# Optimization experiments

Hardware: AMD Instinct MI355X
Metric: run time of the kernel (lower is better)

The kernel has to match this reference:

```python
import jax, jax.numpy as jnp
import numpy as np

V, D, F, B, E = 50257, 1024, 2048, 64, 512  # vocab, embed/rnn dim, fc hidden, batch, entities


def setup_inputs() -> dict:
    key = jax.random.key(0)
    ks = jax.random.split(key, 12)
    s = 0.05
    return {
        "entity_hiddens": jax.random.normal(ks[0], (B, E, D), jnp.float32),
        "question": jax.random.randint(ks[1], (B,), 0, V),
        "keys_mask": jax.random.randint(ks[2], (B, E), 0, 2).astype(bool),
        "emb": jax.random.normal(ks[3], (V, D), jnp.float32) * s,
        "W1": jax.random.normal(ks[4], (D, F), jnp.float32) * s,
        "b1": jnp.zeros((F,), jnp.float32),
        "W2": jax.random.normal(ks[5], (F, D), jnp.float32) * s,
        "b2": jnp.zeros((D,), jnp.float32),
        "A": jax.random.normal(ks[6], (D, D), jnp.float32) * s,  # entity_attn_matrix
        "H": jax.random.normal(ks[7], (D, D), jnp.float32) * s,
        "Ws": jax.random.normal(ks[8], (D, V), jnp.float32) * s,
        "bs": jnp.zeros((V,), jnp.float32),
    }


def reference(entity_hiddens, question, keys_mask, emb, W1, b1, W2, b2, A, H, Ws, bs):
    # embed question token and project: [B, D]
    eq0 = emb[question]
    q = jax.nn.relu(eq0 @ W1 + b1) @ W2 + b2
    # attention_entities actual returned math:
    # reduce_sum(expand_dims(q@A,1) * boolean_mask(entities, mask), axis=1)
    # == (q @ A) * sum over all masked entities (a single [D] vector)
    qA = q @ A  # [B, D]
    m = keys_mask.astype(entity_hiddens.dtype)
    ent_sum = jnp.sum(entity_hiddens * m[..., None], axis=(0, 1))  # [D]
    u = qA * ent_sum  # [B, D]
    logits = (q + u @ H) @ Ws + bs  # [B, V]
    return jax.nn.softmax(logits, axis=-1)
```

## Files before the change

kernel.cpp:

```cpp
#include <hip/hip_runtime.h>
#include <stdint.h>

#define V_ 50257
#define D_ 1024
#define F_ 2048
#define B_ 64
#define E_ 512
#define ROWS_ (B_*E_)

typedef __attribute__((ext_vector_type(8))) short bf16x8;
typedef __attribute__((ext_vector_type(4))) float f32x4;
typedef __attribute__((ext_vector_type(4), aligned(4))) float f32x4a;

__device__ __forceinline__ unsigned rne1(float a) {
  unsigned u = __float_as_uint(a);
  return (u + 0x7FFFu + ((u >> 16) & 1u)) >> 16;
}

__device__ __forceinline__ float waveMax(float v) {
#pragma unroll
  for (int o = 32; o > 0; o >>= 1) v = fmaxf(v, __shfl_xor(v, o, 64));
  return v;
}
__device__ __forceinline__ float waveSum(float v) {
#pragma unroll
  for (int o = 32; o > 0; o >>= 1) v += __shfl_xor(v, o, 64);
  return v;
}


__device__ __forceinline__ void ent_partial_body(int bid, const float* __restrict__ eh,
                                                 const void* __restrict__ mask,
                                                 float* __restrict__ part) {
  __shared__ int s_mode;
  const int tid = threadIdx.x;
  const uint32_t* mu = (const uint32_t*)mask;
  int f = 0;
  for (int i = tid; i < (ROWS_ / 4); i += 256) {
    uint32_t u = mu[i];
    if (u == 0x3F800000u) f |= 2;
    else if (u & 0xFFFFFF00u) f |= 1;
  }
  if (tid == 0) s_mode = 0;
  __syncthreads();
  if (f) atomicOr(&s_mode, f);
  __syncthreads();
  const int sm = s_mode;
  const int mode = (sm & 1) ? 1 : ((sm & 2) ? 2 : 0);

  float4 acc = make_float4(0.f, 0.f, 0.f, 0.f);
  const float4* eh4 = (const float4*)eh;
  for (int row = bid; row < ROWS_; row += 512) {
    bool on;
    if (mode == 1)      on = ((const unsigned char*)mask)[row] != 0;
    else if (mode == 2) on = ((const float*)mask)[row] != 0.f;
    else                on = ((const int*)mask)[row] != 0;
    if (on) {
      float4 v = eh4[(size_t)row * (D_ / 4) + tid];
      acc.x += v.x; acc.y += v.y; acc.z += v.z; acc.w += v.w;
    }
  }
  ((float4*)part)[(size_t)bid * (D_ / 4) + tid] = acc;
}

__device__ __forceinline__ void ent_reduce_body(int bid, const float* __restrict__ part,
                                                float* __restrict__ entsum) {
  int d = bid * 256 + threadIdx.x;
  float s0 = 0.f, s1 = 0.f, s2 = 0.f, s3 = 0.f;
  for (int i = 0; i < 512; i += 4) {
    s0 += part[(size_t)(i    ) * D_ + d];
    s1 += part[(size_t)(i + 1) * D_ + d];
    s2 += part[(size_t)(i + 2) * D_ + d];
    s3 += part[(size_t)(i + 3) * D_ + d];
  }
  entsum[d] = (s0 + s1) + (s2 + s3);
}

__device__ __forceinline__ void gemm64_body(int bx, int by, const float* __restrict__ X,
                                            const int* __restrict__ gatherIdx,
                                            const float* __restrict__ emb,
                                            const float* __restrict__ W,
                                            int K, int N, int KB, float* __restrict__ part) {
  const int l  = threadIdx.x & 63;
  const int rg = __builtin_amdgcn_readfirstlane((int)(threadIdx.x >> 6));
  const int c  = bx * 64 + l;
  const int k0 = by * KB;
  const int m0 = rg * 16;

  const float* Xp = gatherIdx ? emb : X;
  int rb[16];
#pragma unroll
  for (int r = 0; r < 16; ++r) {
    int m = m0 + r;
    rb[r] = gatherIdx ? gatherIdx[m] * K : m * K;
  }

  float acc[16];
#pragma unroll
  for (int r = 0; r < 16; ++r) acc[r] = 0.f;

  for (int k = k0; k < k0 + KB; k += 8) {
    float wv[8];
#pragma unroll
    for (int j = 0; j < 8; ++j) wv[j] = W[(size_t)(k + j) * N + c];
#pragma unroll
    for (int r = 0; r < 16; ++r) {
      float4 x0 = *(const float4*)&Xp[rb[r] + k];
      float4 x1 = *(const float4*)&Xp[rb[r] + k + 4];
      acc[r] = fmaf(x0.x, wv[0], acc[r]);
      acc[r] = fmaf(x0.y, wv[1], acc[r]);
      acc[r] = fmaf(x0.z, wv[2], acc[r]);
      acc[r] = fmaf(x0.w, wv[3], acc[r]);
      acc[r] = fmaf(x1.x, wv[4], acc[r]);
      acc[r] = fmaf(x1.y, wv[5], acc[r]);
      acc[r] = fmaf(x1.z, wv[6], acc[r]);
      acc[r] = fmaf(x1.w, wv[7], acc[r]);
    }
  }
  size_t base = (size_t)by * ((size_t)64 * N);
#pragma unroll
  for (int r = 0; r < 16; ++r) part[base + (size_t)(m0 + r) * N + c] = acc[r];
}

__device__ __forceinline__ void reduce_ep_body(int bid, const float* __restrict__ part,
                                               int nsplit, int MN, int N,
                                               const float* __restrict__ vecB,
                                               const float* __restrict__ addend,
                                               int mode, float* __restrict__ dst,
                                               unsigned short* __restrict__ dhi,
                                               unsigned short* __restrict__ dlo) {
  int idx = bid * 256 + threadIdx.x;
  if (idx >= MN) return;
  float s = 0.f;
  for (int i = 0; i < nsplit; ++i) s += part[(size_t)i * MN + idx];
  int c = idx & (N - 1);
  if (mode == 1)      { s += vecB[c]; s = s > 0.f ? s : 0.f; dst[idx] = s; }
  else if (mode == 2) { s += vecB[c]; dst[idx] = s; }
  else if (mode == 3) { s *= vecB[c]; dst[idx] = s; }
  else {
    s += addend[idx];
    unsigned hi = rne1(s);
    float hif = __uint_as_float(hi << 16);
    dhi[idx] = (unsigned short)hi;
    dlo[idx] = (unsigned short)rne1(s - hif);
  }
}

__global__ void k_p1(const float* __restrict__ eh, const void* __restrict__ mask,
                     float* __restrict__ entpart, const int* __restrict__ ques,
                     const float* __restrict__ emb, const float* __restrict__ W1,
                     float* __restrict__ gpart) {
  int bid = blockIdx.x;
  if (bid < 512) ent_partial_body(bid, eh, mask, entpart);
  else {
    int b2 = bid - 512;
    gemm64_body(b2 & 31, b2 >> 5, nullptr, ques, emb, W1, 1024, 2048, 64, gpart);
  }
}

__global__ void k_p2(const float* __restrict__ entpart, float* __restrict__ entsum,
                     const float* __restrict__ gpart, const float* __restrict__ b1,
                     float* __restrict__ hbuf) {
  int bid = blockIdx.x;
  if (bid < 4) ent_reduce_body(bid, entpart, entsum);
  else reduce_ep_body(bid - 4, gpart, 16, 64 * 2048, 2048, b1, nullptr, 1, hbuf, nullptr, nullptr);
}

__global__ void k_gemm64(const float* __restrict__ X, const float* __restrict__ W,
                         int K, int N, int KB, float* __restrict__ part) {
  gemm64_body(blockIdx.x, blockIdx.y, X, nullptr, nullptr, W, K, N, KB, part);
}

__global__ void k_reduce_ep(const float* __restrict__ part, int nsplit, int MN, int N,
                            const float* __restrict__ vecB, const float* __restrict__ addend,
                            int mode, float* __restrict__ dst,
                            unsigned short* __restrict__ dhi, unsigned short* __restrict__ dlo) {
  reduce_ep_body(blockIdx.x, part, nsplit, MN, N, vecB, addend, mode, dst, dhi, dlo);
}

__global__ __launch_bounds__(512, 1) void k_gemm_big(const unsigned short* __restrict__ zhi,
                                                     const unsigned short* __restrict__ zlo,
                                                     const float* __restrict__ Ws,
                                                     float* __restrict__ part2) {
  __shared__ float lds[2][32 * 516];
  const int t   = threadIdx.x;
  const int l   = t & 63;
  const int w   = t >> 6;
  const int col = l & 15;
  const int g   = l >> 4;
  const int c0  = (blockIdx.x < 98) ? blockIdx.x * 512 : (V_ - 512);
  const int kbase = blockIdx.y * 512;

  const int rr0 = t >> 7;
  const int ccf = (t & 127) * 4;

  unsigned aoff[4];
#pragma unroll
  for (int m = 0; m < 4; ++m) aoff[m] = (unsigned)((m * 16 + col) * D_ + g * 8);

  f32x4 acc[4][4];
#pragma unroll
  for (int n = 0; n < 4; ++n)
#pragma unroll
    for (int m = 0; m < 4; ++m) acc[n][m] = (f32x4){0.f, 0.f, 0.f, 0.f};

  {
    f32x4a gg[8];
#pragma unroll
    for (int r8 = 0; r8 < 8; ++r8) {
      const int r = r8 * 4 + rr0;
      gg[r8] = *(const f32x4a*)(Ws + (size_t)(kbase + r) * V_ + c0 + ccf);
    }
#pragma unroll
    for (int r8 = 0; r8 < 8; ++r8) {
      const int r = r8 * 4 + rr0;
      *(f32x4*)&lds[0][r * 516 + ccf] = (f32x4)gg[r8];
    }
  }
  __syncthreads();

  for (int tt = 0; tt < 16; ++tt) {
    const int buf = tt & 1;
    const int k0  = kbase + tt * 32;

    bf16x8 ah[4], al[4];
#pragma unroll
    for (int m = 0; m < 4; ++m) {
      ah[m] = *(const bf16x8*)(zhi + aoff[m] + k0);
      al[m] = *(const bf16x8*)(zlo + aoff[m] + k0);
    }

    f32x4a gg[8];
    if (tt + 1 < 16) {
      const float* wb = Ws + (size_t)(k0 + 32) * V_ + c0 + ccf;
#pragma unroll
      for (int r8 = 0; r8 < 8; ++r8)
        gg[r8] = *(const f32x4a*)(wb + (size_t)(r8 * 4 + rr0) * V_);
    }
    __builtin_amdgcn_sched_barrier(0);

#pragma unroll
    for (int n = 0; n < 4; ++n) {
      float f[8];
#pragma unroll
      for (int j = 0; j < 8; ++j)
        f[j] = lds[buf][(g * 8 + j) * 516 + w * 64 + n * 16 + col];

      union { bf16x8 v; unsigned u[4]; } bh, bl;
#pragma unroll
      for (int j = 0; j < 4; ++j) {
        unsigned h0 = rne1(f[2 * j]);
        unsigned h1 = rne1(f[2 * j + 1]);
        float h0f = __uint_as_float(h0 << 16);
        float h1f = __uint_as_float(h1 << 16);
        bh.u[j] = h0 | (h1 << 16);
        bl.u[j] = rne1(f[2 * j] - h0f) | (rne1(f[2 * j + 1] - h1f) << 16);
      }
#pragma unroll
      for (int m = 0; m < 4; ++m) acc[n][m] = __builtin_amdgcn_mfma_f32_16x16x32_bf16(ah[m], bh.v, acc[n][m], 0, 0, 0);
#pragma unroll
      for (int m = 0; m < 4; ++m) acc[n][m] = __builtin_amdgcn_mfma_f32_16x16x32_bf16(ah[m], bl.v, acc[n][m], 0, 0, 0);
#pragma unroll
      for (int m = 0; m < 4; ++m) acc[n][m] = __builtin_amdgcn_mfma_f32_16x16x32_bf16(al[m], bh.v, acc[n][m], 0, 0, 0);
    }
    __builtin_amdgcn_sched_barrier(0);

    if (tt + 1 < 16) {
#pragma unroll
      for (int r8 = 0; r8 < 8; ++r8) {
        const int r = r8 * 4 + rr0;
        *(f32x4*)&lds[buf ^ 1][r * 516 + ccf] = (f32x4)gg[r8];
      }
    }
    __syncthreads();
  }

  float* pout = part2 + (size_t)blockIdx.y * ((size_t)64 * V_);
#pragma unroll
  for (int n = 0; n < 4; ++n) {
    const int c = c0 + w * 64 + n * 16 + col;
    if (c < V_) {
#pragma unroll
      for (int m = 0; m < 4; ++m)
#pragma unroll
        for (int i = 0; i < 4; ++i)
          pout[(size_t)(m * 16 + g * 4 + i) * V_ + c] = acc[n][m][i];
    }
  }
}

#define SM_CHUNK 12565

__global__ void k_redbias(const float* __restrict__ part2, const float* __restrict__ bs,
                          float* __restrict__ logits) {
  const int r = blockIdx.x >> 2, q = blockIdx.x & 3;
  const int beg = q * SM_CHUNK;
  const int end = (beg + SM_CHUNK < V_) ? beg + SM_CHUNK : V_;
  const float* p0 = part2 + (size_t)r * V_;
  const float* p1 = part2 + (size_t)64 * V_ + (size_t)r * V_;
  float* orow = logits + (size_t)r * V_;
  for (int i = beg + threadIdx.x; i < end; i += 256) orow[i] = p0[i] + p1[i] + bs[i];
}


__global__ void k_softmax1(const float* __restrict__ logits, float2* __restrict__ stats) {
  __shared__ float smx[4], ssum[4];
  const int r = blockIdx.x >> 2, q = blockIdx.x & 3;
  const int beg = q * SM_CHUNK;
  const int end = (beg + SM_CHUNK < V_) ? beg + SM_CHUNK : V_;
  const float* row = logits + (size_t)r * V_;

  float mx = -3.4e38f;
  for (int i = beg + threadIdx.x; i < end; i += 256) mx = fmaxf(mx, row[i]);
  mx = waveMax(mx);
  if ((threadIdx.x & 63) == 0) smx[threadIdx.x >> 6] = mx;
  __syncthreads();
  mx = fmaxf(fmaxf(smx[0], smx[1]), fmaxf(smx[2], smx[3]));

  float s = 0.f;
  for (int i = beg + threadIdx.x; i < end; i += 256) s += __expf(row[i] - mx);
  s = waveSum(s);
  if ((threadIdx.x & 63) == 0) ssum[threadIdx.x >> 6] = s;
  __syncthreads();
  s = (ssum[0] + ssum[1]) + (ssum[2] + ssum[3]);

  if (threadIdx.x == 0) stats[blockIdx.x] = make_float2(mx, s);
}

__global__ void k_softmax2(const float* __restrict__ logits, const float2* __restrict__ stats,
                           float* __restrict__ out) {
  const int r = blockIdx.x >> 2, q = blockIdx.x & 3;
  float2 s0 = stats[r * 4 + 0], s1 = stats[r * 4 + 1];
  float2 s2 = stats[r * 4 + 2], s3 = stats[r * 4 + 3];
  float M = fmaxf(fmaxf(s0.x, s1.x), fmaxf(s2.x, s3.x));
  float S = s0.y * __expf(s0.x - M) + s1.y * __expf(s1.x - M)
          + s2.y * __expf(s2.x - M) + s3.y * __expf(s3.x - M);
  float inv = 1.f / S;
  const int beg = q * SM_CHUNK;
  const int end = (beg + SM_CHUNK < V_) ? beg + SM_CHUNK : V_;
  const float* row = logits + (size_t)r * V_;
  float* orow = out + (size_t)r * V_;
  for (int i = beg + threadIdx.x; i < end; i += 256) orow[i] = __expf(row[i] - M) * inv;
}

extern "C" void kernel_launch(void* const* d_in, const int* in_sizes, int n_in,
                              void* d_out, int out_size, void* d_ws, size_t ws_size,
                              hipStream_t stream) {
  const float* eh   = (const float*)d_in[0];
  const int*   ques = (const int*)d_in[1];
  const void*  mask = d_in[2];
  const float* emb  = (const float*)d_in[3];
  const float* W1   = (const float*)d_in[4];
  const float* b1   = (const float*)d_in[5];
  const float* W2   = (const float*)d_in[6];
  const float* b2   = (const float*)d_in[7];
  const float* A    = (const float*)d_in[8];
  const float* H    = (const float*)d_in[9];
  const float* Ws   = (const float*)d_in[10];
  const float* bs   = (const float*)d_in[11];
  float* out = (float*)d_out;
  char* ws = (char*)d_ws;

  float*          logits  = (float*)(ws + 0);
  float*          gpart   = (float*)(ws + 0);
  float*          entpart = (float*)(ws + 12866048);
  float*          entsum  = (float*)(ws + 14963200);
  float*          hbuf    = (float*)(ws + 14967296);
  float*          qbuf    = (float*)(ws + 15491584);
  float*          ubuf    = (float*)(ws + 15753728);
  unsigned short* zhi16   = (unsigned short*)(ws + 16015872);
  unsigned short* zlo16   = (unsigned short*)(ws + 16146944);
  float2*         stats   = (float2*)(ws + 16278016);
  float*          part2   = (float*)(ws + 20971520);

  k_p1<<<1024, 256, 0, stream>>>(eh, mask, entpart, ques, emb, W1, gpart);
  k_p2<<<516, 256, 0, stream>>>(entpart, entsum, gpart, b1, hbuf);

  k_gemm64<<<dim3(16, 32), 256, 0, stream>>>(hbuf, W2, 2048, 1024, 64, gpart);
  k_reduce_ep<<<256, 256, 0, stream>>>(gpart, 32, 64 * 1024, 1024, b2, nullptr, 2, qbuf, nullptr, nullptr);

  k_gemm64<<<dim3(16, 16), 256, 0, stream>>>(qbuf, A, 1024, 1024, 64, gpart);
  k_reduce_ep<<<256, 256, 0, stream>>>(gpart, 16, 64 * 1024, 1024, entsum, nullptr, 3, ubuf, nullptr, nullptr);

  k_gemm64<<<dim3(16, 16), 256, 0, stream>>>(ubuf, H, 1024, 1024, 64, gpart);
  k_reduce_ep<<<256, 256, 0, stream>>>(gpart, 16, 64 * 1024, 1024, nullptr, qbuf, 4, nullptr, zhi16, zlo16);

  k_gemm_big<<<dim3(99, 2), 512, 0, stream>>>(zhi16, zlo16, Ws, part2);
  k_redbias<<<256, 256, 0, stream>>>(part2, bs, logits);

  k_softmax1<<<256, 256, 0, stream>>>(logits, stats);
  k_softmax2<<<256, 256, 0, stream>>>(logits, stats, out);

  (void)in_sizes; (void)n_in; (void)out_size; (void)ws_size;
}
```

Baseline: 268.7 us.

## Fuse split-K reduction into softmax, pre-pack A fragments, shrink big GEMM tiles

```diff
diff --git a/kernel.cpp b/kernel.cpp
--- a/kernel.cpp
+++ b/kernel.cpp
@@ -67,6 +67,7 @@
                                                 float* __restrict__ entsum) {
   int d = bid * 256 + threadIdx.x;
   float s0 = 0.f, s1 = 0.f, s2 = 0.f, s3 = 0.f;
+#pragma unroll 8
   for (int i = 0; i < 512; i += 4) {
     s0 += part[(size_t)(i    ) * D_ + d];
     s1 += part[(size_t)(i + 1) * D_ + d];
@@ -122,28 +123,46 @@
   for (int r = 0; r < 16; ++r) part[base + (size_t)(m0 + r) * N + c] = acc[r];
 }
 
-__device__ __forceinline__ void reduce_ep_body(int bid, const float* __restrict__ part,
-                                               int nsplit, int MN, int N,
-                                               const float* __restrict__ vecB,
-                                               const float* __restrict__ addend,
-                                               int mode, float* __restrict__ dst,
-                                               unsigned short* __restrict__ dhi,
-                                               unsigned short* __restrict__ dlo) {
+template<int NSPLIT>
+__device__ __forceinline__ void reduce_body_t(int bid, const float* __restrict__ part,
+                                              int MN, int N,
+                                              const float* __restrict__ vecB,
+                                              const float* __restrict__ addend,
+                                              int mode, float* __restrict__ dst,
+                                              unsigned short* __restrict__ ph,
+                                              unsigned short* __restrict__ pl) {
   int idx = bid * 256 + threadIdx.x;
   if (idx >= MN) return;
+
+  if (mode == 4) {
+    const int d   = idx;
+    const int j   = d & 7;
+    const int l   = (d >> 3) & 63;
+    const int m   = (d >> 9) & 3;
+    const int tg  = d >> 11;
+    const int col = l & 15;
+    const int g   = l >> 4;
+    const int row = m * 16 + col;
+    const int kk  = tg * 32 + g * 8 + j;
+    const int src = row * 1024 + kk;
+    float s = 0.f;
+#pragma unroll
+    for (int i = 0; i < NSPLIT; ++i) s += part[(size_t)i * MN + src];
+    s += addend[src];
+    unsigned hi = rne1(s);
+    float hif = __uint_as_float(hi << 16);
+    ph[d] = (unsigned short)hi;
+    pl[d] = (unsigned short)rne1(s - hif);
+    return;
+  }
+
   float s = 0.f;
-  for (int i = 0; i < nsplit; ++i) s += part[(size_t)i * MN + idx];
+#pragma unroll
+  for (int i = 0; i < NSPLIT; ++i) s += part[(size_t)i * MN + idx];
   int c = idx & (N - 1);
   if (mode == 1)      { s += vecB[c]; s = s > 0.f ? s : 0.f; dst[idx] = s; }
   else if (mode == 2) { s += vecB[c]; dst[idx] = s; }
-  else if (mode == 3) { s *= vecB[c]; dst[idx] = s; }
-  else {
-    s += addend[idx];
-    unsigned hi = rne1(s);
-    float hif = __uint_as_float(hi << 16);
-    dhi[idx] = (unsigned short)hi;
-    dlo[idx] = (unsigned short)rne1(s - hif);
-  }
+  else                { s *= vecB[c]; dst[idx] = s; }
 }
 
 __global__ void k_p1(const float* __restrict__ eh, const void* __restrict__ mask,
@@ -163,7 +182,7 @@
                      float* __restrict__ hbuf) {
   int bid = blockIdx.x;
   if (bid < 4) ent_reduce_body(bid, entpart, entsum);
-  else reduce_ep_body(bid - 4, gpart, 16, 64 * 2048, 2048, b1, nullptr, 1, hbuf, nullptr, nullptr);
+  else reduce_body_t<16>(bid - 4, gpart, 64 * 2048, 2048, b1, nullptr, 1, hbuf, nullptr, nullptr);
 }
 
 __global__ void k_gemm64(const float* __restrict__ X, const float* __restrict__ W,
@@ -171,32 +190,26 @@
   gemm64_body(blockIdx.x, blockIdx.y, X, nullptr, nullptr, W, K, N, KB, part);
 }
 
-__global__ void k_reduce_ep(const float* __restrict__ part, int nsplit, int MN, int N,
-                            const float* __restrict__ vecB, const float* __restrict__ addend,
-                            int mode, float* __restrict__ dst,
-                            unsigned short* __restrict__ dhi, unsigned short* __restrict__ dlo) {
-  reduce_ep_body(blockIdx.x, part, nsplit, MN, N, vecB, addend, mode, dst, dhi, dlo);
-}
-
-__global__ __launch_bounds__(512, 1) void k_gemm_big(const unsigned short* __restrict__ zhi,
-                                                     const unsigned short* __restrict__ zlo,
+template<int NSPLIT>
+__global__ void k_reduce_t(const float* __restrict__ part, int MN, int N,
+                           const float* __restrict__ vecB, const float* __restrict__ addend,
+                           int mode, float* __restrict__ dst,
+                           unsigned short* __restrict__ ph, unsigned short* __restrict__ pl) {
+  reduce_body_t<NSPLIT>(blockIdx.x, part, MN, N, vecB, addend, mode, dst, ph, pl);
+}
+
+__global__ __launch_bounds__(256, 2) void k_gemm_big(const unsigned short* __restrict__ zpkh,
+                                                     const unsigned short* __restrict__ zpkl,
                                                      const float* __restrict__ Ws,
                                                      float* __restrict__ part2) {
-  __shared__ float lds[2][32 * 516];
+  __shared__ float lds[2][32 * 260];
   const int t   = threadIdx.x;
   const int l   = t & 63;
   const int w   = t >> 6;
   const int col = l & 15;
   const int g   = l >> 4;
-  const int c0  = (blockIdx.x < 98) ? blockIdx.x * 512 : (V_ - 512);
+  const int c0  = (blockIdx.x < 196) ? blockIdx.x * 256 : (V_ - 256);
   const int kbase = blockIdx.y * 512;
-
-  const int rr0 = t >> 7;
-  const int ccf = (t & 127) * 4;
-
-  unsigned aoff[4];
-#pragma unroll
-  for (int m = 0; m < 4; ++m) aoff[m] = (unsigned)((m * 16 + col) * D_ + g * 8);
 
   f32x4 acc[4][4];
 #pragma unroll
@@ -207,35 +220,36 @@
   {
     f32x4a gg[8];
 #pragma unroll
-    for (int r8 = 0; r8 < 8; ++r8) {
-      const int r = r8 * 4 + rr0;
-      gg[r8] = *(const f32x4a*)(Ws + (size_t)(kbase + r) * V_ + c0 + ccf);
-    }
-#pragma unroll
-    for (int r8 = 0; r8 < 8; ++r8) {
-      const int r = r8 * 4 + rr0;
-      *(f32x4*)&lds[0][r * 516 + ccf] = (f32x4)gg[r8];
+    for (int i = 0; i < 8; ++i) {
+      const int r = w + 4 * i;
+      gg[i] = *(const f32x4a*)(Ws + (size_t)(kbase + r) * V_ + c0 + 4 * l);
+    }
+#pragma unroll
+    for (int i = 0; i < 8; ++i) {
+      const int r = w + 4 * i;
+      *(f32x4*)&lds[0][r * 260 + 4 * l] = (f32x4)gg[i];
     }
   }
   __syncthreads();
 
   for (int tt = 0; tt < 16; ++tt) {
     const int buf = tt & 1;
-    const int k0  = kbase + tt * 32;
+    const int tg  = (kbase >> 5) + tt;
 
     bf16x8 ah[4], al[4];
 #pragma unroll
     for (int m = 0; m < 4; ++m) {
-      ah[m] = *(const bf16x8*)(zhi + aoff[m] + k0);
-      al[m] = *(const bf16x8*)(zlo + aoff[m] + k0);
+      const int zb = ((tg * 4 + m) * 64 + l) * 8;
+      ah[m] = *(const bf16x8*)(zpkh + zb);
+      al[m] = *(const bf16x8*)(zpkl + zb);
     }
 
     f32x4a gg[8];
     if (tt + 1 < 16) {
-      const float* wb = Ws + (size_t)(k0 + 32) * V_ + c0 + ccf;
-#pragma unroll
-      for (int r8 = 0; r8 < 8; ++r8)
-        gg[r8] = *(const f32x4a*)(wb + (size_t)(r8 * 4 + rr0) * V_);
+      const float* wb = Ws + (size_t)(kbase + (tt + 1) * 32) * V_ + c0 + 4 * l;
+#pragma unroll
+      for (int i = 0; i < 8; ++i)
+        gg[i] = *(const f32x4a*)(wb + (size_t)(w + 4 * i) * V_);
     }
     __builtin_amdgcn_sched_barrier(0);
 
@@ -244,7 +258,7 @@
       float f[8];
 #pragma unroll
       for (int j = 0; j < 8; ++j)
-        f[j] = lds[buf][(g * 8 + j) * 516 + w * 64 + n * 16 + col];
+        f[j] = lds[buf][(g * 8 + j) * 260 + w * 64 + n * 16 + col];
 
       union { bf16x8 v; unsigned u[4]; } bh, bl;
 #pragma unroll
@@ -267,9 +281,9 @@
 
     if (tt + 1 < 16) {
 #pragma unroll
-      for (int r8 = 0; r8 < 8; ++r8) {
-        const int r = r8 * 4 + rr0;
-        *(f32x4*)&lds[buf ^ 1][r * 516 + ccf] = (f32x4)gg[r8];
+      for (int i = 0; i < 8; ++i) {
+        const int r = w + 4 * i;
+        *(f32x4*)&lds[buf ^ 1][r * 260 + 4 * l] = (f32x4)gg[i];
       }
     }
     __syncthreads();
@@ -279,46 +293,34 @@
 #pragma unroll
   for (int n = 0; n < 4; ++n) {
     const int c = c0 + w * 64 + n * 16 + col;
-    if (c < V_) {
-#pragma unroll
-      for (int m = 0; m < 4; ++m)
-#pragma unroll
-        for (int i = 0; i < 4; ++i)
-          pout[(size_t)(m * 16 + g * 4 + i) * V_ + c] = acc[n][m][i];
-    }
+#pragma unroll
+    for (int m = 0; m < 4; ++m)
+#pragma unroll
+      for (int i = 0; i < 4; ++i)
+        pout[(size_t)(m * 16 + g * 4 + i) * V_ + c] = acc[n][m][i];
   }
 }
 
 #define SM_CHUNK 12565
 
-__global__ void k_redbias(const float* __restrict__ part2, const float* __restrict__ bs,
-                          float* __restrict__ logits) {
+__global__ void k_softmax1(const float* __restrict__ part2, const float* __restrict__ bs,
+                           float2* __restrict__ stats) {
+  __shared__ float smx[4], ssum[4];
   const int r = blockIdx.x >> 2, q = blockIdx.x & 3;
   const int beg = q * SM_CHUNK;
   const int end = (beg + SM_CHUNK < V_) ? beg + SM_CHUNK : V_;
   const float* p0 = part2 + (size_t)r * V_;
   const float* p1 = part2 + (size_t)64 * V_ + (size_t)r * V_;
-  float* orow = logits + (size_t)r * V_;
-  for (int i = beg + threadIdx.x; i < end; i += 256) orow[i] = p0[i] + p1[i] + bs[i];
-}
-
-
-__global__ void k_softmax1(const float* __restrict__ logits, float2* __restrict__ stats) {
-  __shared__ float smx[4], ssum[4];
-  const int r = blockIdx.x >> 2, q = blockIdx.x & 3;
-  const int beg = q * SM_CHUNK;
-  const int end = (beg + SM_CHUNK < V_) ? beg + SM_CHUNK : V_;
-  const float* row = logits + (size_t)r * V_;
 
   float mx = -3.4e38f;
-  for (int i = beg + threadIdx.x; i < end; i += 256) mx = fmaxf(mx, row[i]);
+  for (int i = beg + threadIdx.x; i < end; i += 256) mx = fmaxf(mx, p0[i] + p1[i] + bs[i]);
   mx = waveMax(mx);
   if ((threadIdx.x & 63) == 0) smx[threadIdx.x >> 6] = mx;
   __syncthreads();
   mx = fmaxf(fmaxf(smx[0], smx[1]), fmaxf(smx[2], smx[3]));
 
   float s = 0.f;
-  for (int i = beg + threadIdx.x; i < end; i += 256) s += __expf(row[i] - mx);
+  for (int i = beg + threadIdx.x; i < end; i += 256) s += __expf(p0[i] + p1[i] + bs[i] - mx);
   s = waveSum(s);
   if ((threadIdx.x & 63) == 0) ssum[threadIdx.x >> 6] = s;
   __syncthreads();
@@ -327,8 +329,8 @@
   if (threadIdx.x == 0) stats[blockIdx.x] = make_float2(mx, s);
 }
 
-__global__ void k_softmax2(const float* __restrict__ logits, const float2* __restrict__ stats,
-                           float* __restrict__ out) {
+__global__ void k_softmax2(const float* __restrict__ part2, const float* __restrict__ bs,
+                           const float2* __restrict__ stats, float* __restrict__ out) {
   const int r = blockIdx.x >> 2, q = blockIdx.x & 3;
   float2 s0 = stats[r * 4 + 0], s1 = stats[r * 4 + 1];
   float2 s2 = stats[r * 4 + 2], s3 = stats[r * 4 + 3];
@@ -338,9 +340,11 @@
   float inv = 1.f / S;
   const int beg = q * SM_CHUNK;
   const int end = (beg + SM_CHUNK < V_) ? beg + SM_CHUNK : V_;
-  const float* row = logits + (size_t)r * V_;
+  const float* p0 = part2 + (size_t)r * V_;
+  const float* p1 = part2 + (size_t)64 * V_ + (size_t)r * V_;
   float* orow = out + (size_t)r * V_;
-  for (int i = beg + threadIdx.x; i < end; i += 256) orow[i] = __expf(row[i] - M) * inv;
+  for (int i = beg + threadIdx.x; i < end; i += 256)
+    orow[i] = __expf(p0[i] + p1[i] + bs[i] - M) * inv;
 }
 
 extern "C" void kernel_launch(void* const* d_in, const int* in_sizes, int n_in,
@@ -361,15 +365,14 @@
   float* out = (float*)d_out;
   char* ws = (char*)d_ws;
 
-  float*          logits  = (float*)(ws + 0);
   float*          gpart   = (float*)(ws + 0);
   float*          entpart = (float*)(ws + 12866048);
   float*          entsum  = (float*)(ws + 14963200);
   float*          hbuf    = (float*)(ws + 14967296);
   float*          qbuf    = (float*)(ws + 15491584);
   float*          ubuf    = (float*)(ws + 15753728);
-  unsigned short* zhi16   = (unsigned short*)(ws + 16015872);
-  unsigned short* zlo16   = (unsigned short*)(ws + 16146944);
+  unsigned short* zpkh    = (unsigned short*)(ws + 16015872);
+  unsigned short* zpkl    = (unsigned short*)(ws + 16146944);
   float2*         stats   = (float2*)(ws + 16278016);
   float*          part2   = (float*)(ws + 20971520);
 
@@ -377,19 +380,18 @@
   k_p2<<<516, 256, 0, stream>>>(entpart, entsum, gpart, b1, hbuf);
 
   k_gemm64<<<dim3(16, 32), 256, 0, stream>>>(hbuf, W2, 2048, 1024, 64, gpart);
-  k_reduce_ep<<<256, 256, 0, stream>>>(gpart, 32, 64 * 1024, 1024, b2, nullptr, 2, qbuf, nullptr, nullptr);
+  k_reduce_t<32><<<256, 256, 0, stream>>>(gpart, 64 * 1024, 1024, b2, nullptr, 2, qbuf, nullptr, nullptr);
 
   k_gemm64<<<dim3(16, 16), 256, 0, stream>>>(qbuf, A, 1024, 1024, 64, gpart);
-  k_reduce_ep<<<256, 256, 0, stream>>>(gpart, 16, 64 * 1024, 1024, entsum, nullptr, 3, ubuf, nullptr, nullptr);
+  k_reduce_t<16><<<256, 256, 0, stream>>>(gpart, 64 * 1024, 1024, entsum, nullptr, 3, ubuf, nullptr, nullptr);
 
   k_gemm64<<<dim3(16, 16), 256, 0, stream>>>(ubuf, H, 1024, 1024, 64, gpart);
-  k_reduce_ep<<<256, 256, 0, stream>>>(gpart, 16, 64 * 1024, 1024, nullptr, qbuf, 4, nullptr, zhi16, zlo16);
-
-  k_gemm_big<<<dim3(99, 2), 512, 0, stream>>>(zhi16, zlo16, Ws, part2);
-  k_redbias<<<256, 256, 0, stream>>>(part2, bs, logits);
-
-  k_softmax1<<<256, 256, 0, stream>>>(logits, stats);
-  k_softmax2<<<256, 256, 0, stream>>>(logits, stats, out);
+  k_reduce_t<16><<<256, 256, 0, stream>>>(gpart, 64 * 1024, 1024, nullptr, qbuf, 4, nullptr, zpkh, zpkl);
+
+  k_gemm_big<<<dim3(197, 2), 256, 0, stream>>>(zpkh, zpkl, Ws, part2);
+
+  k_softmax1<<<256, 256, 0, stream>>>(part2, bs, stats);
+  k_softmax2<<<256, 256, 0, stream>>>(part2, bs, stats, out);
 
   (void)in_sizes; (void)n_in; (void)out_size; (void)ws_size;
 }
```

Result: faster. 251.7 us (median of 2 runs) (-6.3%).
